# Kernel optimization log

Measured on AMD Instinct MI355X. Metric: run time of the kernel, lower is better.

Reference implementation:

```python
import jax, jax.numpy as jnp
import numpy as np

B, T, E = 4, 2048, 1024
H, D = 16, 64  # n_heads, head_size


def setup_inputs() -> dict:
    key = jax.random.key(0)
    ks = jax.random.split(key, 6)
    s = 0.02
    x = jax.random.normal(ks[0], (B, T, E), dtype=jnp.float32)
    Wq = jax.random.normal(ks[1], (H, E, D), dtype=jnp.float32) * s
    Wk = jax.random.normal(ks[2], (H, E, D), dtype=jnp.float32) * s
    Wv = jax.random.normal(ks[3], (H, E, D), dtype=jnp.float32) * s
    Wp = jax.random.normal(ks[4], (E, E), dtype=jnp.float32) * s
    bp = jnp.zeros((E,), dtype=jnp.float32)
    return {"x": x, "Wq": Wq, "Wk": Wk, "Wv": Wv, "Wp": Wp, "bp": bp}


def reference(x, Wq, Wk, Wv, Wp, bp):
    # Per-head bias-free Q/K/V projections (vectorized over heads)
    q = jnp.einsum('bte,hed->bhtd', x, Wq)
    k = jnp.einsum('bte,hed->bhtd', x, Wk)
    v = jnp.einsum('bte,hed->bhtd', x, Wv)
    scale = 1.0 / jnp.sqrt(jnp.asarray(D, dtype=x.dtype))
    scores = jnp.einsum('bhtd,bhsd->bhts', q, k) * scale  # [B,H,T,T]
    causal = jnp.tril(jnp.ones((T, T), dtype=bool))
    scores = jnp.where(causal, scores, jnp.asarray(-jnp.inf, dtype=scores.dtype))
    attn = jax.nn.softmax(scores, axis=-1)
    out = jnp.einsum('bhts,bhsd->bhtd', attn, v)  # [B,H,T,D]
    # concat heads: 'nh b t c -> b t (nh c)'
    out = out.transpose(0, 2, 1, 3).reshape(B, T, H * D)
    # output projection (dropout p=0.0 is identity)
    return out @ Wp.T + bp
```

## Files before the change

kernel.cpp:

```cpp
#include <hip/hip_runtime.h>

typedef unsigned short u16;
typedef __attribute__((ext_vector_type(8))) short bf16x8;
typedef __attribute__((ext_vector_type(4))) short bf16x4;
typedef __attribute__((ext_vector_type(4))) float f32x4;

__device__ __forceinline__ u16 f2bf(float f) {
  unsigned u = __float_as_uint(f);
  u += 0x7FFFu + ((u >> 16) & 1u);
  return (u16)(u >> 16);
}
__device__ __forceinline__ unsigned pack2(float a, float b) {
  return (unsigned)f2bf(a) | ((unsigned)f2bf(b) << 16);
}
#if __has_builtin(__builtin_amdgcn_cvt_pk_bf16_f32)
typedef __attribute__((ext_vector_type(2))) __bf16 bf16v2;
__device__ __forceinline__ unsigned cvt_pk(float a, float b) {
  bf16v2 v = __builtin_amdgcn_cvt_pk_bf16_f32(a, b);
  return __builtin_bit_cast(unsigned, v);
}
#else
__device__ __forceinline__ unsigned cvt_pk(float a, float b) { return pack2(a, b); }
#endif
__device__ __forceinline__ uint4 pack8(float4 a, float4 b) {
  uint4 r;
  r.x = cvt_pk(a.x, a.y); r.y = cvt_pk(a.z, a.w);
  r.z = cvt_pk(b.x, b.y); r.w = cvt_pk(b.z, b.w);
  return r;
}
__device__ __forceinline__ void gload16(const void* g, void* l) {
  __builtin_amdgcn_global_load_lds(
      (const __attribute__((address_space(1))) void*)g,
      (__attribute__((address_space(3))) void*)l, 16, 0, 0);
}
__device__ __forceinline__ f32x4 mfma16(bf16x4 a, bf16x4 b, f32x4 c) {
#if __has_builtin(__builtin_amdgcn_mfma_f32_16x16x16bf16_1k)
  return __builtin_amdgcn_mfma_f32_16x16x16bf16_1k(a, b, c, 0, 0, 0);
#elif __has_builtin(__builtin_amdgcn_mfma_f32_16x16x16_bf16)
  return __builtin_amdgcn_mfma_f32_16x16x16_bf16(a, b, c, 0, 0, 0);
#else
  asm volatile("v_mfma_f32_16x16x16_bf16 %0, %1, %2, %0\n\ts_nop 2"
               : "+v"(c) : "v"(a), "v"(b));
  return c;
#endif
}

__global__ __launch_bounds__(256) void prep(
    const float* __restrict__ x, u16* __restrict__ xbf,
    const float* __restrict__ Wq, const float* __restrict__ Wk,
    const float* __restrict__ Wv, u16* __restrict__ wt,
    const float* __restrict__ Wp, u16* __restrict__ wpbf) {
  const int tid = threadIdx.x;
  const int b = blockIdx.x;
  __shared__ __align__(16) u16 tile[64 * 72];
  if (b < 4096) {
    const size_t i = (size_t)b * 256 + tid;
    const float4* p = (const float4*)(x + i * 8);
    *(uint4*)(xbf + i * 8) = pack8(p[0], p[1]);
  } else if (b < 4864) {
    const int idx = b - 4096;
    const int w = idx >> 8;
    const int mat = (idx >> 4) & 15;
    const int r0 = (idx & 15) * 64;
    const float* src = (w == 0 ? Wq : (w == 1 ? Wk : Wv)) + (size_t)mat * 1024 * 64;
    u16* dst = wt + (size_t)w * 1024 * 1024 + (size_t)mat * 1024 * 64;
#pragma unroll
    for (int i = 0; i < 2; ++i) {
      const int c = tid + i * 256;
      const int r = c >> 3, off = (c & 7) * 8;
      const float* p = src + (size_t)(r0 + r) * 64 + off;
      *(uint4*)(&tile[r * 72 + off]) = pack8(*(const float4*)p, *(const float4*)(p + 4));
    }
    __syncthreads();
#pragma unroll
    for (int i = 0; i < 2; ++i) {
      const int c = tid + i * 256;
      const int d = c >> 3, roff = (c & 7) * 8;
      bf16x8 v;
#pragma unroll
      for (int j = 0; j < 8; ++j) v[j] = (short)tile[(roff + j) * 72 + d];
      *(bf16x8*)(dst + (size_t)d * 1024 + r0 + roff) = v;
    }
  } else {
    const size_t i = (size_t)(b - 4864) * 256 + tid;
    const float4* p = (const float4*)(Wp + i * 8);
    *(uint4*)(wpbf + i * 8) = pack8(p[0], p[1]);
  }
}

template <int MODE>
__global__ __launch_bounds__(256) void gemm_bt(
    const u16* __restrict__ A, const u16* __restrict__ BT,
    u16* __restrict__ o0, u16* __restrict__ o1, u16* __restrict__ o2,
    float* __restrict__ fout, const float* __restrict__ bp) {
  __shared__ __align__(16) u16 As[2][128 * 32];
  __shared__ __align__(16) u16 Bs[2][128 * 32];
  const int tid = threadIdx.x;
  const int lane = tid & 63, wv = tid >> 6;
  const int g = lane >> 4, ln = lane & 15;
  const int wm = wv >> 1, wn = wv & 1;
  const int m0 = blockIdx.x * 128, n0 = blockIdx.y * 128;

  const f32x4 fz = {0.f, 0.f, 0.f, 0.f};
  f32x4 acc[4][4];
#pragma unroll
  for (int i = 0; i < 4; ++i)
#pragma unroll
    for (int j = 0; j < 4; ++j) acc[i][j] = fz;

  for (int k0 = 0; k0 < 1024; k0 += 64) {
    __syncthreads();
#pragma unroll
    for (int hf = 0; hf < 2; ++hf)
#pragma unroll
      for (int j = 0; j < 2; ++j) {
        const int c = j * 256 + tid;
        const int r = c >> 2, off = (c & 3) * 8;
        gload16(A + (size_t)(m0 + r) * 1024 + k0 + hf * 32 + off, &As[hf][c * 8]);
        gload16(BT + (size_t)(n0 + r) * 1024 + k0 + hf * 32 + off, &Bs[hf][c * 8]);
      }
    __syncthreads();
#pragma unroll
    for (int hf = 0; hf < 2; ++hf) {
      bf16x8 af[4], bfr[4];
#pragma unroll
      for (int rt = 0; rt < 4; ++rt)
        af[rt] = *(const bf16x8*)(&As[hf][(wm * 64 + rt * 16 + ln) * 32 + g * 8]);
#pragma unroll
      for (int ct = 0; ct < 4; ++ct)
        bfr[ct] = *(const bf16x8*)(&Bs[hf][(wn * 64 + ct * 16 + ln) * 32 + g * 8]);
#pragma unroll
      for (int rt = 0; rt < 4; ++rt)
#pragma unroll
        for (int ct = 0; ct < 4; ++ct)
          acc[rt][ct] = __builtin_amdgcn_mfma_f32_16x16x32_bf16(af[rt], bfr[ct],
                                                                acc[rt][ct], 0, 0, 0);
    }
  }

  if (MODE == 0) {
    const int which = n0 >> 10;
    const int nl0 = (n0 & 1023) + wn * 64;
    const float qs = (which == 0) ? 0.1803368801f : 1.0f;
    if (which < 2) {
#pragma unroll
      for (int rt = 0; rt < 4; ++rt)
#pragma unroll
        for (int ct = 0; ct < 4; ++ct) {
          const int nl = nl0 + ct * 16 + ln;
          const int h = nl >> 6, d = nl & 63;
          const unsigned p01 = cvt_pk(acc[rt][ct][0] * qs, acc[rt][ct][1] * qs);
          const unsigned p23 = cvt_pk(acc[rt][ct][2] * qs, acc[rt][ct][3] * qs);
          const u16 vv[4] = {(u16)p01, (u16)(p01 >> 16), (u16)p23, (u16)(p23 >> 16)};
#pragma unroll
          for (int r = 0; r < 4; ++r) {
            const int m = m0 + wm * 64 + rt * 16 + 4 * g + r;
            const int b = m >> 11, t = m & 2047;
            const size_t bh_base = (size_t)(b * 16 + h) * 131072;
            if (which == 0) {
              o0[bh_base + (size_t)t * 64 + d] = vv[r];
            } else {
              o1[bh_base + (size_t)(t >> 6) * 4096 + (d >> 3) * 512 +
                 (t & 63) * 8 + (d & 7)] = vv[r];
            }
          }
        }
    } else {
#pragma unroll
      for (int rt = 0; rt < 4; ++rt) {
        const int tb = m0 + wm * 64 + rt * 16 + 4 * g;
        const int b = tb >> 11, t = tb & 2047;
        const int tile = t >> 6, tl = t & 63;
#pragma unroll
        for (int ct = 0; ct < 4; ++ct) {
          const int nl = nl0 + ct * 16 + ln;
          const int h = nl >> 6, d = nl & 63;
          uint2 pv;
          pv.x = cvt_pk(acc[rt][ct][0], acc[rt][ct][1]);
          pv.y = cvt_pk(acc[rt][ct][2], acc[rt][ct][3]);
          *(uint2*)(o2 + (size_t)(b * 16 + h) * 131072 + (size_t)tile * 4096 +
                    (tl >> 3) * 512 + d * 8 + ((tl >> 2) & 1) * 4) = pv;
        }
      }
    }
  } else {
#pragma unroll
    for (int ct = 0; ct < 4; ++ct) {
      const int n = n0 + wn * 64 + ct * 16 + ln;
      const float bias = bp[n];
#pragma unroll
      for (int rt = 0; rt < 4; ++rt)
#pragma unroll
        for (int r = 0; r < 4; ++r) {
          const int m = m0 + wm * 64 + rt * 16 + 4 * g + r;
          fout[(size_t)m * 1024 + n] = acc[rt][ct][r] + bias;
        }
    }
  }
}

__global__ __launch_bounds__(256) void attn_kernel(
    const u16* __restrict__ Q, const u16* __restrict__ K,
    const u16* __restrict__ VT, u16* __restrict__ AO) {
  const int tid = threadIdx.x;
  const int wv = tid >> 6, lane = tid & 63, g = lane >> 4, ln = lane & 15;
  const int bh = blockIdx.x;
  const int qi = 15 - blockIdx.y;
  const u16* Qb = Q + (size_t)bh * 131072;
  const u16* Kb = K + (size_t)bh * 131072;
  const u16* Vb = VT + (size_t)bh * 131072;

  __shared__ __align__(16) u16 KV[2][2][4096];

  const int b = bh >> 4, h = bh & 15;
  const short ob = 0x3F80;
  const bf16x4 ones = {ob, ob, ob, ob};
  const f32x4 fz = {0.f, 0.f, 0.f, 0.f};

  const int q0 = qi * 128;
  const int nt = 2 * qi + 2;
  const int ntw = 2 * qi + 1 + (wv >> 1);

  const int L0 = tid, L1 = tid + 256;

  bf16x8 qa[2][2];
#pragma unroll
  for (int rt = 0; rt < 2; ++rt) {
    const int row = q0 + wv * 32 + rt * 16 + ln;
#pragma unroll
    for (int hh = 0; hh < 2; ++hh)
      qa[rt][hh] = *(const bf16x8*)(Qb + (size_t)row * 64 + hh * 32 + g * 8);
  }

#define STAGE(buf, tile)                                              \
  {                                                                   \
    const u16* kt_ = Kb + (size_t)(tile) * 4096;                      \
    const u16* vt_ = Vb + (size_t)(tile) * 4096;                      \
    gload16(kt_ + L0 * 8, &KV[buf][0][L0 * 8]);                       \
    gload16(kt_ + L1 * 8, &KV[buf][0][L1 * 8]);                       \
    gload16(vt_ + L0 * 8, &KV[buf][1][L0 * 8]);                       \
    gload16(vt_ + L1 * 8, &KV[buf][1][L1 * 8]);                       \
  }

  STAGE(0, 0);

  f32x4 oacc[2][4], lacc[2];
#pragma unroll
  for (int rt = 0; rt < 2; ++rt) {
    lacc[rt] = fz;
#pragma unroll
    for (int dt = 0; dt < 4; ++dt) oacc[rt][dt] = fz;
  }

  for (int kt = 0; kt < nt; ++kt) {
    __builtin_amdgcn_s_barrier();
    __builtin_amdgcn_sched_barrier(0);
    if (kt + 1 < nt) {
      STAGE((kt + 1) & 1, kt + 1);
      asm volatile("s_waitcnt vmcnt(4)" ::: "memory");
    } else {
      asm volatile("s_waitcnt vmcnt(0)" ::: "memory");
    }
    __builtin_amdgcn_sched_barrier(0);
    __builtin_amdgcn_s_barrier();
    __builtin_amdgcn_sched_barrier(0);
    if (kt < ntw) {
      const int bufi = kt & 1;
      const u16* Ksb = &KV[bufi][0][0];
      const u16* Vsb = &KV[bufi][1][0];
      const int s0 = kt * 64;
      f32x4 sfT[2][4];
#pragma unroll
      for (int st = 0; st < 4; ++st) {
        const bf16x8 kb0 = *(const bf16x8*)(Ksb + (g * 64 + st * 16 + ln) * 8);
        const bf16x8 kb1 =
            *(const bf16x8*)(Ksb + ((g + 4) * 64 + st * 16 + ln) * 8);
#pragma unroll
        for (int rt = 0; rt < 2; ++rt) {
          sfT[rt][st] = __builtin_amdgcn_mfma_f32_16x16x32_bf16(kb0, qa[rt][0],
                                                                fz, 0, 0, 0);
          sfT[rt][st] = __builtin_amdgcn_mfma_f32_16x16x32_bf16(kb1, qa[rt][1],
                                                                sfT[rt][st], 0, 0, 0);
        }
      }
      const bool diag = (kt == ntw - 1);
      bf16x4 pa[2][4];
#pragma unroll
      for (int rt = 0; rt < 2; ++rt) {
        const int qloc = wv * 32 + rt * 16 + ln;
#pragma unroll
        for (int st = 0; st < 4; ++st) {
          float e[4];
#pragma unroll
          for (int r = 0; r < 4; ++r) e[r] = __builtin_amdgcn_exp2f(sfT[rt][st][r]);
          if (diag) {
            const int sloc = s0 - q0 + st * 16 + 4 * g;
#pragma unroll
            for (int r = 0; r < 4; ++r)
              if (sloc + r > qloc) e[r] = 0.f;
          }
          uint2 packed = {cvt_pk(e[0], e[1]), cvt_pk(e[2], e[3])};
          pa[rt][st] = __builtin_bit_cast(bf16x4, packed);
        }
      }
#pragma unroll
      for (int st = 0; st < 4; ++st) {
#pragma unroll
        for (int dt = 0; dt < 4; ++dt) {
          const bf16x4 vb = *(const bf16x4*)(
              Vsb + ((st * 2 + (g >> 1)) * 64 + dt * 16 + ln) * 8 + (g & 1) * 4);
#pragma unroll
          for (int rt = 0; rt < 2; ++rt)
            oacc[rt][dt] = mfma16(pa[rt][st], vb, oacc[rt][dt]);
        }
#pragma unroll
        for (int rt = 0; rt < 2; ++rt)
          lacc[rt] = mfma16(pa[rt][st], ones, lacc[rt]);
      }
    }
  }
#undef STAGE
#pragma unroll
  for (int rt = 0; rt < 2; ++rt) {
    float linv[4];
#pragma unroll
    for (int r = 0; r < 4; ++r) linv[r] = 1.f / lacc[rt][r];
#pragma unroll
    for (int dt = 0; dt < 4; ++dt) {
      const unsigned p01 =
          cvt_pk(oacc[rt][dt][0] * linv[0], oacc[rt][dt][1] * linv[1]);
      const unsigned p23 =
          cvt_pk(oacc[rt][dt][2] * linv[2], oacc[rt][dt][3] * linv[3]);
      const u16 vv[4] = {(u16)p01, (u16)(p01 >> 16), (u16)p23, (u16)(p23 >> 16)};
#pragma unroll
      for (int r = 0; r < 4; ++r) {
        const int qg = q0 + wv * 32 + rt * 16 + 4 * g + r;
        AO[(size_t)(b * 2048 + qg) * 1024 + h * 64 + dt * 16 + ln] = vv[r];
      }
    }
  }
}

extern "C" void kernel_launch(void* const* d_in, const int* in_sizes, int n_in,
                              void* d_out, int out_size, void* d_ws, size_t ws_size,
                              hipStream_t stream) {
  const float* x  = (const float*)d_in[0];
  const float* Wq = (const float*)d_in[1];
  const float* Wk = (const float*)d_in[2];
  const float* Wv = (const float*)d_in[3];
  const float* Wp = (const float*)d_in[4];
  const float* bp = (const float*)d_in[5];
  float* out = (float*)d_out;

  char* ws = (char*)d_ws;
  const size_t MB = 1048576;
  u16* xbf  = (u16*)(ws);
  u16* aows = (u16*)(ws);
  u16* wt   = (u16*)(ws + 16 * MB);
  u16* wpbf = (u16*)(ws + 22 * MB);
  u16* qws  = (u16*)(ws + 24 * MB);
  u16* kws  = (u16*)(ws + 40 * MB);
  u16* vtws = (u16*)(ws + 56 * MB);

  prep<<<dim3(5376), 256, 0, stream>>>(x, xbf, Wq, Wk, Wv, wt, Wp, wpbf);
  gemm_bt<0><<<dim3(64, 24), 256, 0, stream>>>(xbf, wt, qws, kws, vtws,
                                               nullptr, nullptr);
  attn_kernel<<<dim3(64, 16), 256, 0, stream>>>(qws, kws, vtws, aows);
  gemm_bt<1><<<dim3(64, 8), 256, 0, stream>>>(aows, wpbf, nullptr, nullptr,
                                              nullptr, out, bp);
}
```

Baseline: 265.2 us.

## Rewrite projection GEMMs as 8-wave 128x256 tiles with double-buffered prefetch

Both projection GEMMs are replaced by a 512-thread kernel that computes 128x256 output tiles with 8 waves, each owning a 64x64 sub-tile. LDS is double-buffered, so the loads for the next K step are issued before the MFMAs of the current step, with explicit vmcnt waits, barriers and raised priority during MFMA runs. Block IDs are remapped in a grouped order to improve L2 reuse. The aim is to hide global-load latency and reduce syncthreads stalls, at the cost of doubled LDS use (96 KB per block), fewer blocks in flight, and fragile hand-written wait counts.

```diff
diff --git a/kernel.cpp b/kernel.cpp
--- a/kernel.cpp
+++ b/kernel.cpp
@@ -89,17 +89,42 @@
 }
 
 template <int MODE>
-__global__ __launch_bounds__(256) void gemm_bt(
+__global__ __launch_bounds__(512, 2) void gemm8(
     const u16* __restrict__ A, const u16* __restrict__ BT,
     u16* __restrict__ o0, u16* __restrict__ o1, u16* __restrict__ o2,
     float* __restrict__ fout, const float* __restrict__ bp) {
-  __shared__ __align__(16) u16 As[2][128 * 32];
-  __shared__ __align__(16) u16 Bs[2][128 * 32];
+  __shared__ __align__(16) u16 As[2][2][128 * 32];
+  __shared__ __align__(16) u16 Bs[2][2][256 * 32];
   const int tid = threadIdx.x;
-  const int lane = tid & 63, wv = tid >> 6;
-  const int g = lane >> 4, ln = lane & 15;
-  const int wm = wv >> 1, wn = wv & 1;
-  const int m0 = blockIdx.x * 128, n0 = blockIdx.y * 128;
+  const int wid = tid >> 6, lane = tid & 63, g = lane >> 4, ln = lane & 15;
+  const int wr = wid >> 2, wc = wid & 3;
+
+  const int nwg = 64 * gridDim.y;
+  int bid = blockIdx.y * 64 + blockIdx.x;
+  bid = (bid & 7) * (nwg >> 3) + (bid >> 3);
+  const int bx = bid & 63, by = bid >> 6;
+  const int m0 = bx * 128, n0 = by * 256;
+
+  const int cA0 = tid, cA1 = tid + 512;
+  const int rB0 = tid >> 2, oB0 = (tid & 3) * 8;
+  const int rB1 = (tid + 512) >> 2, oB1 = ((tid + 512) & 3) * 8;
+
+#define SA(buf, t_)                                                          \
+  {                                                                          \
+    const int kk = (t_)*64;                                                  \
+    gload16(A + (size_t)(m0 + ((cA0 >> 2) & 127)) * 1024 + kk + (cA0 & 3) * 8, \
+            &As[buf][0][(cA0 & 511) * 8]);                                   \
+    gload16(A + (size_t)(m0 + ((cA1 >> 2) & 127)) * 1024 + kk + 32 +         \
+                (cA1 & 3) * 8,                                               \
+            &As[buf][1][(cA1 & 511) * 8]);                                   \
+  }
+#define SB(buf, t_, kh)                                                      \
+  {                                                                          \
+    const int kk = (t_)*64 + (kh)*32;                                        \
+    gload16(BT + (size_t)(n0 + rB0) * 1024 + kk + oB0, &Bs[buf][kh][tid * 8]); \
+    gload16(BT + (size_t)(n0 + rB1) * 1024 + kk + oB1,                       \
+            &Bs[buf][kh][(tid + 512) * 8]);                                  \
+  }
 
   const f32x4 fz = {0.f, 0.f, 0.f, 0.f};
   f32x4 acc[4][4];
@@ -108,76 +133,109 @@
 #pragma unroll
     for (int j = 0; j < 4; ++j) acc[i][j] = fz;
 
-  for (int k0 = 0; k0 < 1024; k0 += 64) {
-    __syncthreads();
-#pragma unroll
-    for (int hf = 0; hf < 2; ++hf)
-#pragma unroll
-      for (int j = 0; j < 2; ++j) {
-        const int c = j * 256 + tid;
-        const int r = c >> 2, off = (c & 3) * 8;
-        gload16(A + (size_t)(m0 + r) * 1024 + k0 + hf * 32 + off, &As[hf][c * 8]);
-        gload16(BT + (size_t)(n0 + r) * 1024 + k0 + hf * 32 + off, &Bs[hf][c * 8]);
-      }
-    __syncthreads();
-#pragma unroll
-    for (int hf = 0; hf < 2; ++hf) {
-      bf16x8 af[4], bfr[4];
-#pragma unroll
-      for (int rt = 0; rt < 4; ++rt)
-        af[rt] = *(const bf16x8*)(&As[hf][(wm * 64 + rt * 16 + ln) * 32 + g * 8]);
-#pragma unroll
-      for (int ct = 0; ct < 4; ++ct)
-        bfr[ct] = *(const bf16x8*)(&Bs[hf][(wn * 64 + ct * 16 + ln) * 32 + g * 8]);
-#pragma unroll
-      for (int rt = 0; rt < 4; ++rt)
-#pragma unroll
-        for (int ct = 0; ct < 4; ++ct)
-          acc[rt][ct] = __builtin_amdgcn_mfma_f32_16x16x32_bf16(af[rt], bfr[ct],
-                                                                acc[rt][ct], 0, 0, 0);
-    }
-  }
+  SA(0, 0);
+  SB(0, 0, 0);
+  SB(0, 0, 1);
+
+  for (int t = 0; t < 16; ++t) {
+    const int buf = t & 1, nbuf = buf ^ 1;
+    const int tn = (t + 1 < 16) ? t + 1 : 15;
+    SA(nbuf, tn);
+    asm volatile("s_waitcnt vmcnt(4)" ::: "memory");
+    __builtin_amdgcn_sched_barrier(0);
+    __builtin_amdgcn_s_barrier();
+    __builtin_amdgcn_sched_barrier(0);
+    {
+      bf16x8 af[4], bf[4];
+#pragma unroll
+      for (int mi = 0; mi < 4; ++mi)
+        af[mi] = *(const bf16x8*)(&As[buf][0][(wr * 64 + mi * 16 + ln) * 32 + g * 8]);
+#pragma unroll
+      for (int ni = 0; ni < 4; ++ni)
+        bf[ni] = *(const bf16x8*)(&Bs[buf][0][(wc * 64 + ni * 16 + ln) * 32 + g * 8]);
+      asm volatile("s_waitcnt lgkmcnt(0)" ::: "memory");
+      __builtin_amdgcn_sched_barrier(0);
+      __builtin_amdgcn_s_setprio(1);
+#pragma unroll
+      for (int mi = 0; mi < 4; ++mi)
+#pragma unroll
+        for (int ni = 0; ni < 4; ++ni)
+          acc[mi][ni] = __builtin_amdgcn_mfma_f32_16x16x32_bf16(af[mi], bf[ni],
+                                                                acc[mi][ni], 0, 0, 0);
+      __builtin_amdgcn_s_setprio(0);
+    }
+    __builtin_amdgcn_s_barrier();
+    SB(nbuf, tn, 0);
+    SB(nbuf, tn, 1);
+    asm volatile("s_waitcnt vmcnt(6)" ::: "memory");
+    __builtin_amdgcn_sched_barrier(0);
+    __builtin_amdgcn_s_barrier();
+    __builtin_amdgcn_sched_barrier(0);
+    {
+      bf16x8 af[4], bf[4];
+#pragma unroll
+      for (int mi = 0; mi < 4; ++mi)
+        af[mi] = *(const bf16x8*)(&As[buf][1][(wr * 64 + mi * 16 + ln) * 32 + g * 8]);
+#pragma unroll
+      for (int ni = 0; ni < 4; ++ni)
+        bf[ni] = *(const bf16x8*)(&Bs[buf][1][(wc * 64 + ni * 16 + ln) * 32 + g * 8]);
+      asm volatile("s_waitcnt lgkmcnt(0)" ::: "memory");
+      __builtin_amdgcn_sched_barrier(0);
+      __builtin_amdgcn_s_setprio(1);
+#pragma unroll
+      for (int mi = 0; mi < 4; ++mi)
+#pragma unroll
+        for (int ni = 0; ni < 4; ++ni)
+          acc[mi][ni] = __builtin_amdgcn_mfma_f32_16x16x32_bf16(af[mi], bf[ni],
+                                                                acc[mi][ni], 0, 0, 0);
+      __builtin_amdgcn_s_setprio(0);
+    }
+    __builtin_amdgcn_s_barrier();
+  }
+#undef SA
+#undef SB
+  asm volatile("s_waitcnt vmcnt(0)" ::: "memory");
 
   if (MODE == 0) {
-    const int which = n0 >> 10;
-    const int nl0 = (n0 & 1023) + wn * 64;
+    const int which = (n0 + wc * 64) >> 10;
+    const int nl0 = ((n0 + wc * 64) & 1023);
     const float qs = (which == 0) ? 0.1803368801f : 1.0f;
     if (which < 2) {
 #pragma unroll
-      for (int rt = 0; rt < 4; ++rt)
-#pragma unroll
-        for (int ct = 0; ct < 4; ++ct) {
-          const int nl = nl0 + ct * 16 + ln;
+      for (int mi = 0; mi < 4; ++mi)
+#pragma unroll
+        for (int ni = 0; ni < 4; ++ni) {
+          const int nl = nl0 + ni * 16 + ln;
           const int h = nl >> 6, d = nl & 63;
-          const unsigned p01 = cvt_pk(acc[rt][ct][0] * qs, acc[rt][ct][1] * qs);
-          const unsigned p23 = cvt_pk(acc[rt][ct][2] * qs, acc[rt][ct][3] * qs);
+          const unsigned p01 = cvt_pk(acc[mi][ni][0] * qs, acc[mi][ni][1] * qs);
+          const unsigned p23 = cvt_pk(acc[mi][ni][2] * qs, acc[mi][ni][3] * qs);
           const u16 vv[4] = {(u16)p01, (u16)(p01 >> 16), (u16)p23, (u16)(p23 >> 16)};
 #pragma unroll
           for (int r = 0; r < 4; ++r) {
-            const int m = m0 + wm * 64 + rt * 16 + 4 * g + r;
-            const int b = m >> 11, t = m & 2047;
+            const int m = m0 + wr * 64 + mi * 16 + 4 * g + r;
+            const int b = m >> 11, tt = m & 2047;
             const size_t bh_base = (size_t)(b * 16 + h) * 131072;
             if (which == 0) {
-              o0[bh_base + (size_t)t * 64 + d] = vv[r];
+              o0[bh_base + (size_t)tt * 64 + d] = vv[r];
             } else {
-              o1[bh_base + (size_t)(t >> 6) * 4096 + (d >> 3) * 512 +
-                 (t & 63) * 8 + (d & 7)] = vv[r];
+              o1[bh_base + (size_t)(tt >> 6) * 4096 + (d >> 3) * 512 +
+                 (tt & 63) * 8 + (d & 7)] = vv[r];
             }
           }
         }
     } else {
 #pragma unroll
-      for (int rt = 0; rt < 4; ++rt) {
-        const int tb = m0 + wm * 64 + rt * 16 + 4 * g;
-        const int b = tb >> 11, t = tb & 2047;
-        const int tile = t >> 6, tl = t & 63;
-#pragma unroll
-        for (int ct = 0; ct < 4; ++ct) {
-          const int nl = nl0 + ct * 16 + ln;
+      for (int mi = 0; mi < 4; ++mi) {
+        const int tb = m0 + wr * 64 + mi * 16 + 4 * g;
+        const int b = tb >> 11, tt = tb & 2047;
+        const int tile = tt >> 6, tl = tt & 63;
+#pragma unroll
+        for (int ni = 0; ni < 4; ++ni) {
+          const int nl = nl0 + ni * 16 + ln;
           const int h = nl >> 6, d = nl & 63;
           uint2 pv;
-          pv.x = cvt_pk(acc[rt][ct][0], acc[rt][ct][1]);
-          pv.y = cvt_pk(acc[rt][ct][2], acc[rt][ct][3]);
+          pv.x = cvt_pk(acc[mi][ni][0], acc[mi][ni][1]);
+          pv.y = cvt_pk(acc[mi][ni][2], acc[mi][ni][3]);
           *(uint2*)(o2 + (size_t)(b * 16 + h) * 131072 + (size_t)tile * 4096 +
                     (tl >> 3) * 512 + d * 8 + ((tl >> 2) & 1) * 4) = pv;
         }
@@ -185,15 +243,15 @@
     }
   } else {
 #pragma unroll
-    for (int ct = 0; ct < 4; ++ct) {
-      const int n = n0 + wn * 64 + ct * 16 + ln;
+    for (int ni = 0; ni < 4; ++ni) {
+      const int n = n0 + wc * 64 + ni * 16 + ln;
       const float bias = bp[n];
 #pragma unroll
-      for (int rt = 0; rt < 4; ++rt)
+      for (int mi = 0; mi < 4; ++mi)
 #pragma unroll
         for (int r = 0; r < 4; ++r) {
-          const int m = m0 + wm * 64 + rt * 16 + 4 * g + r;
-          fout[(size_t)m * 1024 + n] = acc[rt][ct][r] + bias;
+          const int m = m0 + wr * 64 + mi * 16 + 4 * g + r;
+          fout[(size_t)m * 1024 + n] = acc[mi][ni][r] + bias;
         }
     }
   }
@@ -363,9 +421,9 @@
   u16* vtws = (u16*)(ws + 56 * MB);
 
   prep<<<dim3(5376), 256, 0, stream>>>(x, xbf, Wq, Wk, Wv, wt, Wp, wpbf);
-  gemm_bt<0><<<dim3(64, 24), 256, 0, stream>>>(xbf, wt, qws, kws, vtws,
-                                               nullptr, nullptr);
+  gemm8<0><<<dim3(64, 12), 512, 0, stream>>>(xbf, wt, qws, kws, vtws,
+                                             nullptr, nullptr);
   attn_kernel<<<dim3(64, 16), 256, 0, stream>>>(qws, kws, vtws, aows);
-  gemm_bt<1><<<dim3(64, 8), 256, 0, stream>>>(aows, wpbf, nullptr, nullptr,
-                                              nullptr, out, bp);
-}
+  gemm8<1><<<dim3(64, 4), 512, 0, stream>>>(aows, wpbf, nullptr, nullptr,
+                                            nullptr, out, bp);
+}
```

Measured after the change: 285.4 us. 7.6% more time.
